# Kernel tuning notes

Measured on AMD Instinct MI355X. Metric: run time of the kernel, lower is better.

## Reference

```python
import jax, jax.numpy as jnp
import numpy as np

N_NODES = 100000
IN_FEATURES = 5000
OUT_FEATURES = 64
NNZ = 4000000


def setup_inputs() -> dict:
    key = jax.random.key(0)
    k_row, k_col, k_val, k_w, k_b = jax.random.split(key, 5)
    rows = jax.random.randint(k_row, (NNZ,), 0, N_NODES, dtype=jnp.int64 if jax.config.jax_enable_x64 else jnp.int32)
    cols = jax.random.randint(k_col, (NNZ,), 0, IN_FEATURES, dtype=rows.dtype)
    index = jnp.stack([rows, cols], axis=0)  # [2, nnz] COO
    value = jax.random.uniform(k_val, (NNZ,), dtype=jnp.float32)
    # kaiming_uniform_(mode='fan_out', a=sqrt(5)) on [in, out]: fan_out = out_features
    gain = np.sqrt(2.0 / (1.0 + 5.0))
    bound_w = gain * np.sqrt(3.0 / OUT_FEATURES)
    weight = jax.random.uniform(k_w, (IN_FEATURES, OUT_FEATURES), jnp.float32, -bound_w, bound_w)
    bound_b = 1.0 / np.sqrt(OUT_FEATURES)
    bias = jax.random.uniform(k_b, (OUT_FEATURES,), jnp.float32, -bound_b, bound_b)
    return {"index": index, "value": value, "n": N_NODES, "weight": weight, "bias": bias}


def reference(index, value, n, weight, bias):
    # spmm: out[r, :] = sum over nnz with row==r of value * weight[col, :]
    rows, cols = index[0], index[1]
    contrib = value[:, None] * weight[cols]            # [nnz, out] gather + scale
    res = jax.ops.segment_sum(contrib, rows, num_segments=n)  # [n, out] scatter-add
    return res + bias[None, :]
```

## Files before the change

kernel.cpp:

```cpp
#include <hip/hip_runtime.h>


#define NBF 1024
#define DMAX 128
#define CH 4096
#define CC2 768
#define SP_T 512

__device__ __forceinline__ void ds_fadd(float* p, float v) {
    unsigned a = (unsigned)(unsigned long long)p;
    asm volatile("ds_add_f32 %0, %1" :: "v"(a), "v"(v) : "memory");
}

__global__ void k_init(int* __restrict__ cursorF, int* __restrict__ ovfCnt, int slots) {
    cursorF[threadIdx.x] = threadIdx.x * slots;
    if (threadIdx.x == 0) *ovfCnt = 0;
}

__global__ __launch_bounds__(1024) void k_bin_fixed(const int* __restrict__ rows,
        const int* __restrict__ cols, const float* __restrict__ vals, int nnz,
        unsigned M, int S, int d, int slots, int* __restrict__ cursorF,
        unsigned long long* __restrict__ pairs1, int* __restrict__ ovfCnt,
        unsigned long long* __restrict__ ovf) {
    __shared__ unsigned long long stage[CH];
    __shared__ int histF[NBF], scF[NBF], adjF[NBF];
    __shared__ int wsum[16];
    int t = threadIdx.x, lane = t & 63, wv = t >> 6;
    long long base = (long long)blockIdx.x * CH;
    int count = (int)min((long long)CH, (long long)nnz - base);
    histF[t] = 0;
    __syncthreads();
    int f4[4], rk4[4];
    unsigned long long pk4[4];
#pragma unroll
    for (int k = 0; k < 4; ++k) {
        int i = t + (k << 10);
        f4[k] = -1;
        if (i < count) {
            unsigned r = (unsigned)rows[base + i];
            int c = cols[base + i];
            float vv = vals[base + i];
            int f = (int)(((unsigned long long)r * M) >> S);
            int lr = (int)r - f * d;
            f4[k] = f;
            rk4[k] = atomicAdd(&histF[f], 1);
            pk4[k] = ((unsigned long long)__float_as_uint(vv) << 32) |
                     ((unsigned)f << 20) | ((unsigned)lr << 13) | (unsigned)c;
        }
    }
    __syncthreads();
    int v = histF[t], x = v;
#pragma unroll
    for (int off = 1; off < 64; off <<= 1) {
        int y = __shfl_up(x, off, 64);
        if (lane >= off) x += y;
    }
    if (lane == 63) wsum[wv] = x;
    __syncthreads();
    if (t < 16) {
        int s = wsum[t], xs = s;
#pragma unroll
        for (int off = 1; off < 16; off <<= 1) {
            int y = __shfl_up(xs, off, 16);
            if (t >= off) xs += y;
        }
        wsum[t] = xs - s;
    }
    __syncthreads();
    int incl = x + wsum[wv];
    scF[t] = incl;
    if (v > 0) {
        int g = atomicAdd(&cursorF[t], v);
        adjF[t] = g - (incl - v);
    }
    __syncthreads();
#pragma unroll
    for (int k = 0; k < 4; ++k)
        if (f4[k] >= 0) stage[(scF[f4[k]] - histF[f4[k]]) + rk4[k]] = pk4[k];
    __syncthreads();
    for (int i = t; i < count; i += 1024) {
        unsigned long long p = stage[i];
        int f = (int)((p >> 20) & 1023);
        int dest = adjF[f] + i;
        if (dest < (f + 1) * slots) pairs1[dest] = p;
        else ovf[atomicAdd(ovfCnt, 1)] = p;
    }
}

__global__ __launch_bounds__(SP_T, 8) void k_spmm8(
        const unsigned long long* __restrict__ pairs, const int* __restrict__ cursorF,
        const int* __restrict__ ovfCnt, const unsigned long long* __restrict__ ovf,
        const float* __restrict__ weight, const float* __restrict__ bias,
        float* __restrict__ out, int d, int n, int slots) {
    __shared__ unsigned long long stg[2][CC2];
    __shared__ int histR[2][DMAX], scR[2][DMAX];
    extern __shared__ float acc[];
    int b = blockIdx.x, t = threadIdx.x;
    int row0 = b * d;
    if (row0 >= n) return;
    int nrows = min(d, n - row0);
    long long sbase = (long long)b * slots;
    int cnt = cursorF[b] - (int)sbase;
    if (cnt > slots) cnt = slots;
    if (cnt < 0) cnt = 0;

    for (int i = t; i < (nrows << 6); i += SP_T) acc[i] = 0.0f;
    int g = t >> 4, fq = t & 15;
    int nt = (cnt + CC2 - 1) / CC2;

    int lr2[2], rk2[2];
    unsigned long long pk2[2];

    if (t < DMAX) { histR[0][t] = 0; histR[1][t] = 0; }
    __syncthreads();
    if (nt > 0) {
        int c0 = min(CC2, cnt);
#pragma unroll
        for (int k = 0; k < 2; ++k) {
            int i = t + (k << 9);
            lr2[k] = -1;
            if (i < c0) {
                unsigned long long p = pairs[sbase + i];
                int lr = (int)((p >> 13) & 127);
                lr2[k] = lr; rk2[k] = atomicAdd(&histR[0][lr], 1); pk2[k] = p;
            }
        }
        __syncthreads();
        if (t < 64) {
            int v0 = histR[0][t], v1 = histR[0][t + 64];
            int x0 = v0;
#pragma unroll
            for (int off = 1; off < 64; off <<= 1) {
                int y = __shfl_up(x0, off, 64);
                if (t >= off) x0 += y;
            }
            int tot = __shfl(x0, 63, 64);
            int x1 = v1;
#pragma unroll
            for (int off = 1; off < 64; off <<= 1) {
                int y = __shfl_up(x1, off, 64);
                if (t >= off) x1 += y;
            }
            x1 += tot;
            scR[0][t] = x0; scR[0][t + 64] = x1;
        }
        __syncthreads();
#pragma unroll
        for (int k = 0; k < 2; ++k)
            if (lr2[k] >= 0) stg[0][scR[0][lr2[k]] - histR[0][lr2[k]] + rk2[k]] = pk2[k];
        __syncthreads();
    }

    for (int c = 0; c < nt; ++c) {
        int cur = c & 1, nxt = cur ^ 1;
        bool more = (c + 1 < nt);
        if (more) {
            int nb = (c + 1) * CC2;
            int ncnt = min(CC2, cnt - nb);
#pragma unroll
            for (int k = 0; k < 2; ++k) {
                int i = t + (k << 9);
                lr2[k] = -1;
                if (i < ncnt) {
                    unsigned long long p = pairs[sbase + nb + i];
                    int lr = (int)((p >> 13) & 127);
                    lr2[k] = lr; rk2[k] = atomicAdd(&histR[nxt][lr], 1); pk2[k] = p;
                }
            }
        } else {
            lr2[0] = lr2[1] = -1;
        }
        for (int r = g; r < nrows; r += 32) {
            int e = scR[cur][r], s = e - histR[cur][r];
            if (s >= e) continue;
            float4 a = {0.0f, 0.0f, 0.0f, 0.0f};
            int j = s;
            for (; j + 4 <= e; j += 4) {
                unsigned long long p0 = stg[cur][j + 0];
                unsigned long long p1 = stg[cur][j + 1];
                unsigned long long p2 = stg[cur][j + 2];
                unsigned long long p3 = stg[cur][j + 3];
                const float4 w0 = *(const float4*)(weight + (((int)(p0 & 8191)) << 6) + (fq << 2));
                const float4 w1 = *(const float4*)(weight + (((int)(p1 & 8191)) << 6) + (fq << 2));
                const float4 w2 = *(const float4*)(weight + (((int)(p2 & 8191)) << 6) + (fq << 2));
                const float4 w3 = *(const float4*)(weight + (((int)(p3 & 8191)) << 6) + (fq << 2));
                float v0 = __uint_as_float((unsigned)(p0 >> 32));
                float v1 = __uint_as_float((unsigned)(p1 >> 32));
                float v2 = __uint_as_float((unsigned)(p2 >> 32));
                float v3 = __uint_as_float((unsigned)(p3 >> 32));
                a.x = fmaf(v0, w0.x, a.x); a.y = fmaf(v0, w0.y, a.y);
                a.z = fmaf(v0, w0.z, a.z); a.w = fmaf(v0, w0.w, a.w);
                a.x = fmaf(v1, w1.x, a.x); a.y = fmaf(v1, w1.y, a.y);
                a.z = fmaf(v1, w1.z, a.z); a.w = fmaf(v1, w1.w, a.w);
                a.x = fmaf(v2, w2.x, a.x); a.y = fmaf(v2, w2.y, a.y);
                a.z = fmaf(v2, w2.z, a.z); a.w = fmaf(v2, w2.w, a.w);
                a.x = fmaf(v3, w3.x, a.x); a.y = fmaf(v3, w3.y, a.y);
                a.z = fmaf(v3, w3.z, a.z); a.w = fmaf(v3, w3.w, a.w);
            }
            for (; j < e; ++j) {
                unsigned long long p = stg[cur][j];
                float vv = __uint_as_float((unsigned)(p >> 32));
                const float4 w = *(const float4*)(weight + (((int)(p & 8191)) << 6) + (fq << 2));
                a.x = fmaf(vv, w.x, a.x); a.y = fmaf(vv, w.y, a.y);
                a.z = fmaf(vv, w.z, a.z); a.w = fmaf(vv, w.w, a.w);
            }
            float4* ap = (float4*)&acc[(r << 6) + (fq << 2)];
            float4 o = *ap;
            o.x += a.x; o.y += a.y; o.z += a.z; o.w += a.w;
            *ap = o;
        }
        __syncthreads();
        if (more && t < 64) {
            int v0 = histR[nxt][t], v1 = histR[nxt][t + 64];
            int x0 = v0;
#pragma unroll
            for (int off = 1; off < 64; off <<= 1) {
                int y = __shfl_up(x0, off, 64);
                if (t >= off) x0 += y;
            }
            int tot = __shfl(x0, 63, 64);
            int x1 = v1;
#pragma unroll
            for (int off = 1; off < 64; off <<= 1) {
                int y = __shfl_up(x1, off, 64);
                if (t >= off) x1 += y;
            }
            x1 += tot;
            scR[nxt][t] = x0; scR[nxt][t + 64] = x1;
        }
        __syncthreads();
#pragma unroll
        for (int k = 0; k < 2; ++k)
            if (lr2[k] >= 0) stg[nxt][scR[nxt][lr2[k]] - histR[nxt][lr2[k]] + rk2[k]] = pk2[k];
        if (t < DMAX) histR[cur][t] = 0;
        __syncthreads();
    }

    int oc = *ovfCnt;
    if (oc > 0) {
        __syncthreads();
        for (int i = g; i < oc; i += (SP_T >> 4)) {
            unsigned long long p = ovf[i];
            if ((int)((p >> 20) & 1023) == b) {
                int lr = (int)((p >> 13) & 127);
                int cc = (int)(p & 8191);
                float vv = __uint_as_float((unsigned)(p >> 32));
                const float4 w = *(const float4*)(weight + (cc << 6) + (fq << 2));
                float* ap = &acc[(lr << 6) + (fq << 2)];
                ds_fadd(ap + 0, vv * w.x); ds_fadd(ap + 1, vv * w.y);
                ds_fadd(ap + 2, vv * w.z); ds_fadd(ap + 3, vv * w.w);
            }
        }
        asm volatile("s_waitcnt lgkmcnt(0)" ::: "memory");
        __builtin_amdgcn_sched_barrier(0);
    }
    __syncthreads();

    for (int i = t; i < (nrows << 6); i += SP_T)
        out[((long long)row0 << 6) + i] = acc[i] + bias[i & 63];
}

extern "C" void kernel_launch(void* const* d_in, const int* in_sizes, int n_in,
                              void* d_out, int out_size, void* d_ws, size_t ws_size,
                              hipStream_t stream) {
    const int*   index  = (const int*)d_in[0];
    const float* value  = (const float*)d_in[1];
    const float* weight = (const float*)d_in[3];
    const float* bias   = (const float*)d_in[4];
    float*       out    = (float*)d_out;

    int nnz = in_sizes[0] / 2;
    int n   = out_size / 64;
    const int* rows = index;
    const int* cols = index + nnz;

    int d = (n + NBF - 1) / NBF;
    unsigned M = 0;
    int S = 0;
    for (S = 20; S <= 40; ++S) {
        unsigned long long m = ((1ull << S) + (unsigned)d - 1) / (unsigned)d;
        unsigned long long e = m * (unsigned long long)d - (1ull << S);
        if (m <= 0xffffffffull && e * (unsigned long long)(n > 0 ? n - 1 : 0) < (1ull << S)) {
            M = (unsigned)m;
            break;
        }
    }

    int nChunks = (nnz + CH - 1) / CH;
    char* ws = (char*)d_ws;
    int* cursorF = (int*)ws;
    int* ovfCnt  = (int*)(ws + 4096);
    unsigned long long* pairsS = (unsigned long long*)(ws + 65536);

    size_t szOvf = (((size_t)nnz * 8) + 255) & ~(size_t)255;
    size_t availS = (ws_size > 65536 + szOvf) ? (ws_size - 65536 - szOvf) : 0;
    long long slotsL = (long long)(availS / ((size_t)NBF * 8));
    int slots = (int)(slotsL > 6144 ? 6144 : slotsL);
    if (slots > 64) slots &= ~63;
    if (slots < 1) slots = 1;
    unsigned long long* ovf = (unsigned long long*)(ws + 65536 + (size_t)slots * NBF * 8);

    k_init<<<1, 1024, 0, stream>>>(cursorF, ovfCnt, slots);
    k_bin_fixed<<<nChunks, 1024, 0, stream>>>(rows, cols, value, nnz, M, S, d, slots,
                                              cursorF, pairsS, ovfCnt, ovf);
    size_t smem = (size_t)d * 64 * sizeof(float);
    k_spmm8<<<NBF, SP_T, smem, stream>>>(pairsS, cursorF, ovfCnt, ovf, weight, bias,
                                         out, d, n, slots);
}
```

Measured before the change: 185.1 us.

## Replace double-buffered SpMM staging with single larger chunk and pad bin cursors

The SpMM kernel drops its double-buffered 768-entry staging, where the next chunk's loads overlapped the current chunk's compute. It now uses one 1536-entry stage per iteration with three loads per thread, which means fewer chunk iterations and barriers but no overlap between loading and compute. Separately, the per-bin cursors are spaced 16 ints apart so global atomics from the binning kernel land on different cache lines. The workspace offsets are shifted to make room for the padded cursors.

```diff
diff --git a/kernel.cpp b/kernel.cpp
--- a/kernel.cpp
+++ b/kernel.cpp
@@ -4,8 +4,9 @@
 #define NBF 1024
 #define DMAX 128
 #define CH 4096
-#define CC2 768
+#define CC 1536
 #define SP_T 512
+#define CSTR 16
 
 __device__ __forceinline__ void ds_fadd(float* p, float v) {
     unsigned a = (unsigned)(unsigned long long)p;
@@ -13,7 +14,7 @@
 }
 
 __global__ void k_init(int* __restrict__ cursorF, int* __restrict__ ovfCnt, int slots) {
-    cursorF[threadIdx.x] = threadIdx.x * slots;
+    cursorF[threadIdx.x * CSTR] = threadIdx.x * slots;
     if (threadIdx.x == 0) *ovfCnt = 0;
 }
 
@@ -70,7 +71,7 @@
     int incl = x + wsum[wv];
     scF[t] = incl;
     if (v > 0) {
-        int g = atomicAdd(&cursorF[t], v);
+        int g = atomicAdd(&cursorF[t * CSTR], v);
         adjF[t] = g - (incl - v);
     }
     __syncthreads();
@@ -87,99 +88,73 @@
     }
 }
 
-__global__ __launch_bounds__(SP_T, 8) void k_spmm8(
+__global__ __launch_bounds__(SP_T, 8) void k_spmm9(
         const unsigned long long* __restrict__ pairs, const int* __restrict__ cursorF,
         const int* __restrict__ ovfCnt, const unsigned long long* __restrict__ ovf,
         const float* __restrict__ weight, const float* __restrict__ bias,
         float* __restrict__ out, int d, int n, int slots) {
-    __shared__ unsigned long long stg[2][CC2];
-    __shared__ int histR[2][DMAX], scR[2][DMAX];
+    __shared__ unsigned long long stage[CC];
+    __shared__ int histR[DMAX], scR[DMAX];
     extern __shared__ float acc[];
     int b = blockIdx.x, t = threadIdx.x;
     int row0 = b * d;
     if (row0 >= n) return;
     int nrows = min(d, n - row0);
     long long sbase = (long long)b * slots;
-    int cnt = cursorF[b] - (int)sbase;
+    int cnt = cursorF[b * CSTR] - (int)sbase;
     if (cnt > slots) cnt = slots;
     if (cnt < 0) cnt = 0;
 
     for (int i = t; i < (nrows << 6); i += SP_T) acc[i] = 0.0f;
+
     int g = t >> 4, fq = t & 15;
-    int nt = (cnt + CC2 - 1) / CC2;
-
-    int lr2[2], rk2[2];
-    unsigned long long pk2[2];
-
-    if (t < DMAX) { histR[0][t] = 0; histR[1][t] = 0; }
-    __syncthreads();
-    if (nt > 0) {
-        int c0 = min(CC2, cnt);
-#pragma unroll
-        for (int k = 0; k < 2; ++k) {
+    for (int cb = 0; cb < cnt; cb += CC) {
+        int ccnt = min(CC, cnt - cb);
+        if (t < DMAX) histR[t] = 0;
+        __syncthreads();
+        int lr3[3], rk3[3];
+        unsigned long long pk3[3];
+#pragma unroll
+        for (int k = 0; k < 3; ++k) {
             int i = t + (k << 9);
-            lr2[k] = -1;
-            if (i < c0) {
-                unsigned long long p = pairs[sbase + i];
+            lr3[k] = -1;
+            if (i < ccnt) {
+                unsigned long long p = pairs[sbase + cb + i];
                 int lr = (int)((p >> 13) & 127);
-                lr2[k] = lr; rk2[k] = atomicAdd(&histR[0][lr], 1); pk2[k] = p;
-            }
-        }
-        __syncthreads();
-        if (t < 64) {
-            int v0 = histR[0][t], v1 = histR[0][t + 64];
-            int x0 = v0;
+                lr3[k] = lr;
+                rk3[k] = atomicAdd(&histR[lr], 1);
+                pk3[k] = p;
+            }
+        }
+        __syncthreads();
+        if (t < DMAX) {
+            int v = histR[t], x = v;
+            int lane = t & 63;
 #pragma unroll
             for (int off = 1; off < 64; off <<= 1) {
-                int y = __shfl_up(x0, off, 64);
-                if (t >= off) x0 += y;
-            }
-            int tot = __shfl(x0, 63, 64);
-            int x1 = v1;
-#pragma unroll
-            for (int off = 1; off < 64; off <<= 1) {
-                int y = __shfl_up(x1, off, 64);
-                if (t >= off) x1 += y;
-            }
-            x1 += tot;
-            scR[0][t] = x0; scR[0][t + 64] = x1;
-        }
-        __syncthreads();
-#pragma unroll
-        for (int k = 0; k < 2; ++k)
-            if (lr2[k] >= 0) stg[0][scR[0][lr2[k]] - histR[0][lr2[k]] + rk2[k]] = pk2[k];
-        __syncthreads();
-    }
-
-    for (int c = 0; c < nt; ++c) {
-        int cur = c & 1, nxt = cur ^ 1;
-        bool more = (c + 1 < nt);
-        if (more) {
-            int nb = (c + 1) * CC2;
-            int ncnt = min(CC2, cnt - nb);
-#pragma unroll
-            for (int k = 0; k < 2; ++k) {
-                int i = t + (k << 9);
-                lr2[k] = -1;
-                if (i < ncnt) {
-                    unsigned long long p = pairs[sbase + nb + i];
-                    int lr = (int)((p >> 13) & 127);
-                    lr2[k] = lr; rk2[k] = atomicAdd(&histR[nxt][lr], 1); pk2[k] = p;
-                }
-            }
-        } else {
-            lr2[0] = lr2[1] = -1;
-        }
+                int y = __shfl_up(x, off, 64);
+                if (lane >= off) x += y;
+            }
+            scR[t] = x;
+        }
+        __syncthreads();
+        if (t >= 64 && t < DMAX) scR[t] += scR[63];
+        __syncthreads();
+#pragma unroll
+        for (int k = 0; k < 3; ++k)
+            if (lr3[k] >= 0) stage[(scR[lr3[k]] - histR[lr3[k]]) + rk3[k]] = pk3[k];
+        __syncthreads();
+
         for (int r = g; r < nrows; r += 32) {
-            int e = scR[cur][r], s = e - histR[cur][r];
+            int e = scR[r], s = e - histR[r];
             if (s >= e) continue;
             float4 a = {0.0f, 0.0f, 0.0f, 0.0f};
             int j = s;
             for (; j + 4 <= e; j += 4) {
-                unsigned long long p0 = stg[cur][j + 0];
-                unsigned long long p1 = stg[cur][j + 1];
-                unsigned long long p2 = stg[cur][j + 2];
-                unsigned long long p3 = stg[cur][j + 3];
+                unsigned long long p0 = stage[j + 0];
+                unsigned long long p1 = stage[j + 1];
+                unsigned long long p2 = stage[j + 2];
+                unsigned long long p3 = stage[j + 3];
                 const float4 w0 = *(const float4*)(weight + (((int)(p0 & 8191)) << 6) + (fq << 2));
                 const float4 w1 = *(const float4*)(weight + (((int)(p1 & 8191)) << 6) + (fq << 2));
                 const float4 w2 = *(const float4*)(weight + (((int)(p2 & 8191)) << 6) + (fq << 2));
@@ -198,7 +173,7 @@
                 a.z = fmaf(v3, w3.z, a.z); a.w = fmaf(v3, w3.w, a.w);
             }
             for (; j < e; ++j) {
-                unsigned long long p = stg[cur][j];
+                unsigned long long p = stage[j];
                 float vv = __uint_as_float((unsigned)(p >> 32));
                 const float4 w = *(const float4*)(weight + (((int)(p & 8191)) << 6) + (fq << 2));
                 a.x = fmaf(vv, w.x, a.x); a.y = fmaf(vv, w.y, a.y);
@@ -209,30 +184,6 @@
             o.x += a.x; o.y += a.y; o.z += a.z; o.w += a.w;
             *ap = o;
         }
-        __syncthreads();
-        if (more && t < 64) {
-            int v0 = histR[nxt][t], v1 = histR[nxt][t + 64];
-            int x0 = v0;
-#pragma unroll
-            for (int off = 1; off < 64; off <<= 1) {
-                int y = __shfl_up(x0, off, 64);
-                if (t >= off) x0 += y;
-            }
-            int tot = __shfl(x0, 63, 64);
-            int x1 = v1;
-#pragma unroll
-            for (int off = 1; off < 64; off <<= 1) {
-                int y = __shfl_up(x1, off, 64);
-                if (t >= off) x1 += y;
-            }
-            x1 += tot;
-            scR[nxt][t] = x0; scR[nxt][t + 64] = x1;
-        }
-        __syncthreads();
-#pragma unroll
-        for (int k = 0; k < 2; ++k)
-            if (lr2[k] >= 0) stg[nxt][scR[nxt][lr2[k]] - histR[nxt][lr2[k]] + rk2[k]] = pk2[k];
-        if (t < DMAX) histR[cur][t] = 0;
         __syncthreads();
     }
 
@@ -253,8 +204,8 @@
         }
         asm volatile("s_waitcnt lgkmcnt(0)" ::: "memory");
         __builtin_amdgcn_sched_barrier(0);
-    }
-    __syncthreads();
+        __syncthreads();
+    }
 
     for (int i = t; i < (nrows << 6); i += SP_T)
         out[((long long)row0 << 6) + i] = acc[i] + bias[i & 63];
@@ -289,21 +240,21 @@
     int nChunks = (nnz + CH - 1) / CH;
     char* ws = (char*)d_ws;
     int* cursorF = (int*)ws;
-    int* ovfCnt  = (int*)(ws + 4096);
-    unsigned long long* pairsS = (unsigned long long*)(ws + 65536);
+    int* ovfCnt  = (int*)(ws + (64 << 10));
+    unsigned long long* pairsS = (unsigned long long*)(ws + (128 << 10));
 
     size_t szOvf = (((size_t)nnz * 8) + 255) & ~(size_t)255;
-    size_t availS = (ws_size > 65536 + szOvf) ? (ws_size - 65536 - szOvf) : 0;
+    size_t availS = (ws_size > (128 << 10) + szOvf) ? (ws_size - (128 << 10) - szOvf) : 0;
     long long slotsL = (long long)(availS / ((size_t)NBF * 8));
     int slots = (int)(slotsL > 6144 ? 6144 : slotsL);
     if (slots > 64) slots &= ~63;
     if (slots < 1) slots = 1;
-    unsigned long long* ovf = (unsigned long long*)(ws + 65536 + (size_t)slots * NBF * 8);
+    unsigned long long* ovf = (unsigned long long*)(ws + (128 << 10) + (size_t)slots * NBF * 8);
 
     k_init<<<1, 1024, 0, stream>>>(cursorF, ovfCnt, slots);
     k_bin_fixed<<<nChunks, 1024, 0, stream>>>(rows, cols, value, nnz, M, S, d, slots,
                                               cursorF, pairsS, ovfCnt, ovf);
     size_t smem = (size_t)d * 64 * sizeof(float);
-    k_spmm8<<<NBF, SP_T, smem, stream>>>(pairsS, cursorF, ovfCnt, ovf, weight, bias,
+    k_spmm9<<<NBF, SP_T, smem, stream>>>(pairsS, cursorF, ovfCnt, ovf, weight, bias,
                                          out, d, n, slots);
 }
```

Result: slower. 196.1 us (+6.0%).
